# Performance work log

Measured on AMD Instinct MI355X. Metric: run time of the kernel, lower is better.

The kernel has to match this reference:

```python
import jax, jax.numpy as jnp
import numpy as np

N_NODES = 50000
N_EDGES = 600000
D_FEAT = 128
HIDDEN = 128
N_STEPS = 4


def setup_inputs() -> dict:
    key = jax.random.key(0)
    ks = jax.random.split(key, 10)
    node = jax.random.normal(ks[0], (N_NODES, D_FEAT), dtype=jnp.float32)
    edges = jax.random.randint(ks[1], (2, N_EDGES), 0, N_NODES, dtype=jnp.int64)
    edges_attr = jax.random.uniform(ks[2], (N_EDGES,), dtype=jnp.float32)
    s = 1.0 / np.sqrt(HIDDEN)
    W1 = jax.random.normal(ks[3], (D_FEAT, HIDDEN), dtype=jnp.float32) * s
    b1 = jnp.zeros((HIDDEN,), dtype=jnp.float32)
    Ws = jax.random.normal(ks[4], (N_STEPS, HIDDEN, HIDDEN), dtype=jnp.float32) * s
    bs = jnp.zeros((N_STEPS, HIDDEN), dtype=jnp.float32)
    Wfc = jax.random.normal(ks[5], (HIDDEN, 2), dtype=jnp.float32) * s
    bfc = jnp.zeros((2,), dtype=jnp.float32)
    return {"node": node, "edges": edges, "edges_attr": edges_attr,
            "W1": W1, "b1": b1, "Ws": Ws, "bs": bs, "Wfc": Wfc, "bfc": bfc}


def _gcn_norm(edges, edges_attr, n_nodes):
    # PyG gcn_norm with add_self_loops=True (fill 1.0)
    loop = jnp.arange(n_nodes, dtype=edges.dtype)
    row = jnp.concatenate([edges[0], loop])  # source
    col = jnp.concatenate([edges[1], loop])  # target
    ew = jnp.concatenate([edges_attr, jnp.ones((n_nodes,), dtype=edges_attr.dtype)])
    deg = jax.ops.segment_sum(ew, col, num_segments=n_nodes)
    dinv = jnp.where(deg > 0, jax.lax.rsqrt(jnp.where(deg > 0, deg, 1.0)), 0.0)
    norm = dinv[row] * ew * dinv[col]  # [E+N]
    return row, col, norm


def _gcn_conv(x, row, col, norm, W, b, n_nodes):
    h = x @ W                               # [N, H]
    msg = h[row] * norm[:, None]            # gather + scale [E+N, H]
    agg = jax.ops.segment_sum(msg, col, num_segments=n_nodes)  # scatter-add
    return agg + b


def reference(node, edges, edges_attr, W1, b1, Ws, bs, Wfc, bfc):
    n_nodes = node.shape[0]
    row, col, norm = _gcn_norm(edges, edges_attr, n_nodes)
    x = jax.nn.relu(_gcn_conv(node, row, col, norm, W1, b1, n_nodes))
    for i in range(Ws.shape[0]):
        x_res = x
        x = _gcn_conv(x, row, col, norm, Ws[i], bs[i], n_nodes)
        x = jax.nn.relu(x + x_res)  # residual=True
    x = x @ Wfc + bfc               # [N, 2]
    return jnp.mean(x, axis=0, keepdims=True)  # global_mean_pool(batch=None) -> [1, 2]
```

## Files before the change

kernel.cpp:

```cpp
#include <hip/hip_runtime.h>

#define N_NODES 50000
#define N_EDGES 600000
#define HID 128
#define NCOPY 8
#define NPART 3125

typedef __attribute__((ext_vector_type(8))) short bf16x8;
typedef __attribute__((ext_vector_type(8))) unsigned short u16x8;
typedef __attribute__((ext_vector_type(4))) float f32x4;
typedef __attribute__((ext_vector_type(2))) float f32x2;

__device__ __forceinline__ float bf2f(unsigned short u) {
    return __uint_as_float(((unsigned int)u) << 16);
}
__device__ __forceinline__ unsigned short f2bf(float f) {
    unsigned int u = __float_as_uint(f);
    u = (u + 0x7FFFu + ((u >> 16) & 1u)) >> 16;
    return (unsigned short)u;
}

__device__ __forceinline__ unsigned char fp8enc_hw(float f) {
    return (unsigned char)(__builtin_amdgcn_cvt_pk_fp8_f32(f, f, 0, false) & 0xff);
}


__global__ __launch_bounds__(256) void init_k(unsigned long long* degcnt8, float* cs,
                                              int2* epk_pad,
                                              const float* __restrict__ W1,
                                              const float* __restrict__ Ws,
                                              unsigned short* __restrict__ Wt_hi,
                                              unsigned short* __restrict__ Wt_lo,
                                              int total) {
    int i = blockIdx.x * 256 + threadIdx.x;
    if (i < total) degcnt8[i] = (i < N_NODES) ? (1ull << 32) : 0ull;
    if (i < HID) cs[i] = 0.0f;
    if (i < 8) epk_pad[i] = make_int2(0, 0);
    if (i < 5 * 16384) {
        int l = i >> 14;
        int r = i & 16383;
        int n = r >> 7;
        int k = r & 127;
        const float* src = (l == 0) ? W1 : (Ws + (size_t)(l - 1) * 16384);
        float w = src[k * 128 + n];
        unsigned short hi = f2bf(w);
        unsigned short lo = f2bf(w - bf2f(hi));
        Wt_hi[i] = hi;
        Wt_lo[i] = lo;
    }
}

__global__ __launch_bounds__(256) void edge_deg_k(const int* __restrict__ edges,
                                                  const float* __restrict__ attr,
                                                  unsigned long long* degcnt8,
                                                  int* __restrict__ rank) {
    int e = blockIdx.x * 256 + threadIdx.x;
    int copy = blockIdx.x & (NCOPY - 1);
    if (e < N_EDGES) {
        int c = edges[N_EDGES + e];
        unsigned long long enc = (1ull << 43) +
            (unsigned long long)llrintf(attr[e] * 4294967296.0f);
        unsigned long long old = atomicAdd(&degcnt8[(size_t)copy * N_NODES + c], enc);
        rank[e] = (int)(old >> 43);
    }
}

__global__ __launch_bounds__(256) void scan1_k(const unsigned long long* __restrict__ degcnt8,
                                               int* offs, int* bsum, float* dinv,
                                               int* __restrict__ cbase, int n) {
    __shared__ int s[256];
    int tid = threadIdx.x;
    int i = blockIdx.x * 256 + tid;
    int v = 0;
    if (i < n) {
        unsigned long long attrsum = 0;
        int running = 0;
        #pragma unroll
        for (int c = 0; c < NCOPY; ++c) {
            unsigned long long dc = degcnt8[(size_t)c * n + i];
            cbase[i * NCOPY + c] = running;
            running += (int)(dc >> 43);
            attrsum += dc & ((1ull << 43) - 1);
        }
        v = running;
        float deg = (float)attrsum * (1.0f / 4294967296.0f);
        dinv[i] = rsqrtf(deg);
    }
    s[tid] = v; __syncthreads();
    for (int d = 1; d < 256; d <<= 1) {
        int t = (tid >= d) ? s[tid - d] : 0;
        __syncthreads();
        s[tid] += t;
        __syncthreads();
    }
    if (i < n) offs[i] = s[tid] - v;
    if (tid == 255) bsum[blockIdx.x] = s[255];
}

__global__ __launch_bounds__(256) void scan3_k(int* offs, const int* __restrict__ bsum,
                                               int* cbase, int n, int nb) {
    __shared__ int s[256];
    int tid = threadIdx.x;
    int bv = (tid < nb) ? bsum[tid] : 0;
    s[tid] = bv; __syncthreads();
    for (int d = 1; d < 256; d <<= 1) {
        int t = (tid >= d) ? s[tid - d] : 0;
        __syncthreads();
        s[tid] += t;
        __syncthreads();
    }
    int b = blockIdx.x;
    int pbase = s[b] - bsum[b];
    int i = b * 256 + tid;
    if (i < n) {
        int v = offs[i] + pbase;
        offs[i] = v;
        #pragma unroll
        for (int c = 0; c < NCOPY; ++c) cbase[i * NCOPY + c] += v;
    }
}

__global__ __launch_bounds__(256) void fill_k(const int* __restrict__ edges,
                                              const float* __restrict__ attr,
                                              const float* __restrict__ dinv,
                                              const int* __restrict__ cbase,
                                              const int* __restrict__ rank,
                                              int2* __restrict__ epk) {
    int e = blockIdx.x * 256 + threadIdx.x;
    int copy = blockIdx.x & (NCOPY - 1);
    if (e < N_EDGES) {
        int r = edges[e];
        int c = edges[N_EDGES + e];
        float w = dinv[r] * attr[e] * dinv[c];
        epk[cbase[c * NCOPY + copy] + rank[e]] = make_int2(r, __float_as_int(w));
    }
}


template <bool FP32A>
__global__ __launch_bounds__(256) void mfma_gemm_k(const void* __restrict__ Av,
                                                   const unsigned short* __restrict__ Bh,
                                                   const unsigned short* __restrict__ Bl,
                                                   unsigned char* __restrict__ H, int nrows) {
    int wid  = threadIdx.x >> 6;
    int lane = threadIdx.x & 63;
    int row0 = blockIdx.x * 256 + wid * 64;
    int rl = lane & 15;
    int kg = lane >> 4;

    bf16x8 af[4][4];
    #pragma unroll
    for (int rt = 0; rt < 4; ++rt) {
        int row = row0 + rt * 16 + rl;
        int ar  = row < nrows ? row : nrows - 1;
        #pragma unroll
        for (int kt = 0; kt < 4; ++kt) {
            if (FP32A) {
                const float* Af = (const float*)Av;
                float4 v0 = *(const float4*)(Af + (size_t)ar * HID + kt * 32 + kg * 8);
                float4 v1 = *(const float4*)(Af + (size_t)ar * HID + kt * 32 + kg * 8 + 4);
                bf16x8 t;
                t[0] = (short)f2bf(v0.x); t[1] = (short)f2bf(v0.y);
                t[2] = (short)f2bf(v0.z); t[3] = (short)f2bf(v0.w);
                t[4] = (short)f2bf(v1.x); t[5] = (short)f2bf(v1.y);
                t[6] = (short)f2bf(v1.z); t[7] = (short)f2bf(v1.w);
                af[rt][kt] = t;
            } else {
                const unsigned short* Ab = (const unsigned short*)Av;
                af[rt][kt] = *(const bf16x8*)(Ab + (size_t)ar * HID + kt * 32 + kg * 8);
            }
        }
    }

    f32x4 acc[4][8];
    #pragma unroll
    for (int rt = 0; rt < 4; ++rt)
        #pragma unroll
        for (int nt = 0; nt < 8; ++nt) acc[rt][nt] = (f32x4){0.f, 0.f, 0.f, 0.f};

    #pragma unroll
    for (int nt = 0; nt < 8; ++nt) {
        #pragma unroll
        for (int kt = 0; kt < 4; ++kt) {
            size_t boff = (size_t)(nt * 16 + rl) * HID + kt * 32 + kg * 8;
            bf16x8 bh = *(const bf16x8*)(Bh + boff);
            bf16x8 bl = *(const bf16x8*)(Bl + boff);
            #pragma unroll
            for (int rt = 0; rt < 4; ++rt) {
                acc[rt][nt] = __builtin_amdgcn_mfma_f32_16x16x32_bf16(af[rt][kt], bh, acc[rt][nt], 0, 0, 0);
                acc[rt][nt] = __builtin_amdgcn_mfma_f32_16x16x32_bf16(af[rt][kt], bl, acc[rt][nt], 0, 0, 0);
            }
        }
    }

    #pragma unroll
    for (int rt = 0; rt < 4; ++rt) {
        #pragma unroll
        for (int nt = 0; nt < 8; ++nt) {
            #pragma unroll
            for (int r = 0; r < 4; ++r) {
                int orow = row0 + rt * 16 + kg * 4 + r;
                if (orow < nrows)
                    H[(size_t)orow * HID + nt * 16 + rl] = fp8enc_hw(acc[rt][nt][r]);
            }
        }
    }
}


__device__ __forceinline__ void dec_fma8_pk(uint2 q, float wt, f32x2* a) {
    f32x2 w2 = {wt, wt};
    a[0] += __builtin_amdgcn_cvt_pk_f32_fp8((int)q.x, false) * w2;
    a[1] += __builtin_amdgcn_cvt_pk_f32_fp8((int)q.x, true)  * w2;
    a[2] += __builtin_amdgcn_cvt_pk_f32_fp8((int)q.y, false) * w2;
    a[3] += __builtin_amdgcn_cvt_pk_f32_fp8((int)q.y, true)  * w2;
}

template <bool FINAL>
__global__ __launch_bounds__(256) void aggregate_k(const unsigned char* __restrict__ h,
                                                   const int* __restrict__ offs,
                                                   const int2* __restrict__ epk,
                                                   const float* __restrict__ dinv,
                                                   const float* __restrict__ bias,
                                                   const unsigned short* __restrict__ xprev,
                                                   unsigned short* __restrict__ xout,
                                                   float* __restrict__ part, int n) {
    int tid  = threadIdx.x;
    int wave = (blockIdx.x * 256 + tid) >> 6;
    int lane = tid & 63;
    int g  = lane >> 4;
    int ci = (lane & 15) * 8;
    int w = wave * 4 + g;
    int wc = w < n ? w : n - 1;

    f32x2 a[4];
    #pragma unroll
    for (int j = 0; j < 4; ++j) a[j] = (f32x2){0.f, 0.f};

    int e0 = 0, e1 = 0;
    if (w < n) {
        e0 = offs[w];
        e1 = (w + 1 < n) ? offs[w + 1] : N_EDGES;
    }

    for (int e = e0; e < e1; e += 8) {
        int2 pk[8];
        uint2 q[8];
        #pragma unroll
        for (int u = 0; u < 8; ++u) pk[u] = epk[e + u];
        #pragma unroll
        for (int u = 0; u < 8; ++u) {
            int row = (e + u < e1) ? pk[u].x : wc;
            q[u] = *(const uint2*)(h + (size_t)row * HID + ci);
        }
        #pragma unroll
        for (int u = 0; u < 8; ++u) {
            float wt = (e + u < e1) ? __int_as_float(pk[u].y) : 0.f;
            dec_fma8_pk(q[u], wt, a);
        }
    }

    float av[8];
    #pragma unroll
    for (int j = 0; j < 8; ++j) av[j] = 0.f;

    if (w < n) {
        float di = dinv[w];
        uint2 qw = *(const uint2*)(h + (size_t)w * HID + ci);
        dec_fma8_pk(qw, di * di, a);
        av[0] = a[0][0]; av[1] = a[0][1]; av[2] = a[1][0]; av[3] = a[1][1];
        av[4] = a[2][0]; av[5] = a[2][1]; av[6] = a[3][0]; av[7] = a[3][1];
        float4 b0 = *(const float4*)(bias + ci);
        float4 b1 = *(const float4*)(bias + ci + 4);
        av[0] += b0.x; av[1] += b0.y; av[2] += b0.z; av[3] += b0.w;
        av[4] += b1.x; av[5] += b1.y; av[6] += b1.z; av[7] += b1.w;
        if (xprev) {
            u16x8 xp = *(const u16x8*)(xprev + (size_t)w * HID + ci);
            #pragma unroll
            for (int j = 0; j < 8; ++j) av[j] += bf2f(xp[j]);
        }
        u16x8 o;
        #pragma unroll
        for (int j = 0; j < 8; ++j) {
            av[j] = fmaxf(av[j], 0.f);
            o[j] = f2bf(av[j]);
        }
        *(u16x8*)(xout + (size_t)w * HID + ci) = o;
    }

    if constexpr (FINAL) {
        #pragma unroll
        for (int j = 0; j < 8; ++j) av[j] += __shfl_xor(av[j], 16);
        #pragma unroll
        for (int j = 0; j < 8; ++j) av[j] += __shfl_xor(av[j], 32);
        __shared__ float sw[4][16][8];
        int wv = tid >> 6;
        if (lane < 16) {
            #pragma unroll
            for (int j = 0; j < 8; ++j) sw[wv][lane][j] = av[j];
        }
        __syncthreads();
        if (tid < 128) {
            int l16 = tid >> 3, j = tid & 7;
            part[(size_t)tid * NPART + blockIdx.x] =
                sw[0][l16][j] + sw[1][l16][j] + sw[2][l16][j] + sw[3][l16][j];
        }
    }
}


__global__ __launch_bounds__(256) void head_reduce_k(const float* __restrict__ part,
                                                     float* __restrict__ cs) {
    int col = blockIdx.x;
    float s = 0.f;
    for (int i = threadIdx.x; i < NPART; i += 256)
        s += part[(size_t)col * NPART + i];
    #pragma unroll
    for (int d = 1; d < 64; d <<= 1) s += __shfl_xor(s, d);
    __shared__ float sw[4];
    int lane = threadIdx.x & 63, wv = threadIdx.x >> 6;
    if (lane == 0) sw[wv] = s;
    __syncthreads();
    if (threadIdx.x == 0) cs[col] = sw[0] + sw[1] + sw[2] + sw[3];
}

__global__ __launch_bounds__(128) void final_k(const float* __restrict__ cs,
                                               const float* __restrict__ Wfc,
                                               const float* __restrict__ bfc,
                                               float* __restrict__ out) {
    __shared__ float s0[128], s1[128];
    int k = threadIdx.x;
    float c = cs[k];
    s0[k] = c * Wfc[k * 2 + 0];
    s1[k] = c * Wfc[k * 2 + 1];
    __syncthreads();
    for (int d = 64; d > 0; d >>= 1) {
        if (k < d) { s0[k] += s0[k + d]; s1[k] += s1[k + d]; }
        __syncthreads();
    }
    if (k == 0) {
        out[0] = s0[0] / (float)N_NODES + bfc[0];
        out[1] = s1[0] / (float)N_NODES + bfc[1];
    }
}


extern "C" void kernel_launch(void* const* d_in, const int* in_sizes, int n_in,
                              void* d_out, int out_size, void* d_ws, size_t ws_size,
                              hipStream_t stream) {
    const float* node  = (const float*)d_in[0];
    const int*   edges = (const int*)d_in[1];
    const float* attr  = (const float*)d_in[2];
    const float* W1    = (const float*)d_in[3];
    const float* b1    = (const float*)d_in[4];
    const float* Ws    = (const float*)d_in[5];
    const float* bs    = (const float*)d_in[6];
    const float* Wfc   = (const float*)d_in[7];
    const float* bfc   = (const float*)d_in[8];
    float* out = (float*)d_out;

    char* ws = (char*)d_ws;
    const size_t BN = (size_t)N_NODES * HID * 2;
    unsigned char*  h8     = (unsigned char*)(ws);
    unsigned short* xa_bf  = (unsigned short*)(ws + BN);
    unsigned short* xb_bf  = (unsigned short*)(ws + 2 * BN);
    char* p = ws + 3 * BN;
    unsigned long long* degcnt8 = (unsigned long long*)p; p += (size_t)NCOPY * N_NODES * 8;
    float* dinv  = (float*)p;            p += N_NODES * 4;
    int*   offs  = (int*)p;              p += N_NODES * 4;
    int*   cbase = (int*)p;              p += (size_t)N_NODES * NCOPY * 4;
    int*   rank  = (int*)p;              p += (size_t)N_EDGES * 4;
    int*   bsum  = (int*)p;              p += 1024;
    int2*  epk   = (int2*)p;             p += (size_t)(N_EDGES + 8) * 8;
    float* cs    = (float*)p;            p += 512;
    float* part  = (float*)p;            p += (size_t)128 * NPART * 4;
    unsigned short* wt_hi = (unsigned short*)p;  p += 5 * 16384 * 2;
    unsigned short* wt_lo = (unsigned short*)p;  p += 5 * 16384 * 2;

    const int NB_N  = (N_NODES + 255) / 256;
    const int NB_N8 = (NCOPY * N_NODES + 255) / 256;
    const int NB_E  = (N_EDGES + 255) / 256;

    hipLaunchKernelGGL(init_k,    dim3(NB_N8), dim3(256), 0, stream, degcnt8, cs,
                       epk + N_EDGES, W1, Ws, wt_hi, wt_lo, NCOPY * N_NODES);
    hipLaunchKernelGGL(edge_deg_k,dim3(NB_E),  dim3(256), 0, stream, edges, attr, degcnt8, rank);
    hipLaunchKernelGGL(scan1_k,   dim3(NB_N),  dim3(256), 0, stream, degcnt8, offs, bsum, dinv, cbase, N_NODES);
    hipLaunchKernelGGL(scan3_k,   dim3(NB_N),  dim3(256), 0, stream, offs, bsum, cbase, N_NODES, NB_N);
    hipLaunchKernelGGL(fill_k,    dim3(NB_E),  dim3(256), 0, stream, edges, attr, dinv, cbase, rank, epk);

    const int GB = (N_NODES + 255) / 256;
    const int AB = NPART;

    hipLaunchKernelGGL((mfma_gemm_k<true>), dim3(GB), dim3(256), 0, stream,
                       (const void*)node, wt_hi, wt_lo, h8, N_NODES);
    hipLaunchKernelGGL((aggregate_k<false>), dim3(AB), dim3(256), 0, stream, h8, offs, epk, dinv,
                       b1, (const unsigned short*)nullptr, xa_bf, part, N_NODES);

    unsigned short* xc = xa_bf;
    unsigned short* xn = xb_bf;
    for (int i = 0; i < 4; ++i) {
        hipLaunchKernelGGL((mfma_gemm_k<false>), dim3(GB), dim3(256), 0, stream,
                           (const void*)xc, wt_hi + (size_t)(i + 1) * 16384,
                           wt_lo + (size_t)(i + 1) * 16384, h8, N_NODES);
        if (i < 3) {
            hipLaunchKernelGGL((aggregate_k<false>), dim3(AB), dim3(256), 0, stream, h8, offs, epk, dinv,
                               bs + (size_t)i * HID, xc, xn, part, N_NODES);
        } else {
            hipLaunchKernelGGL((aggregate_k<true>), dim3(AB), dim3(256), 0, stream, h8, offs, epk, dinv,
                               bs + (size_t)i * HID, xc, xn, part, N_NODES);
        }
        unsigned short* t = xc; xc = xn; xn = t;
    }

    hipLaunchKernelGGL(head_reduce_k, dim3(128), dim3(256), 0, stream, part, cs);
    hipLaunchKernelGGL(final_k,       dim3(1),   dim3(128), 0, stream, cs, Wfc, bfc, out);
}
```

Baseline: 248.8 us.

## Degree-sort node processing order and pack edge records into 32 bits

```diff
diff --git a/kernel.cpp b/kernel.cpp
--- a/kernel.cpp
+++ b/kernel.cpp
@@ -1,4 +1,5 @@
 #include <hip/hip_runtime.h>
+#include <hip/hip_fp16.h>
 
 #define N_NODES 50000
 #define N_EDGES 600000
@@ -26,7 +27,7 @@
 
 
 __global__ __launch_bounds__(256) void init_k(unsigned long long* degcnt8, float* cs,
-                                              int2* epk_pad,
+                                              int* hist, unsigned* epk_pad,
                                               const float* __restrict__ W1,
                                               const float* __restrict__ Ws,
                                               unsigned short* __restrict__ Wt_hi,
@@ -35,7 +36,8 @@
     int i = blockIdx.x * 256 + threadIdx.x;
     if (i < total) degcnt8[i] = (i < N_NODES) ? (1ull << 32) : 0ull;
     if (i < HID) cs[i] = 0.0f;
-    if (i < 8) epk_pad[i] = make_int2(0, 0);
+    if (i < 256) hist[i] = 0;
+    if (i < 8) epk_pad[i] = 0u;
     if (i < 5 * 16384) {
         int l = i >> 14;
         int r = i & 16383;
@@ -67,7 +69,8 @@
 
 __global__ __launch_bounds__(256) void scan1_k(const unsigned long long* __restrict__ degcnt8,
                                                int* offs, int* bsum, float* dinv,
-                                               int* __restrict__ cbase, int n) {
+                                               int* __restrict__ cbase,
+                                               int* __restrict__ dcnt, int* hist, int n) {
     __shared__ int s[256];
     int tid = threadIdx.x;
     int i = blockIdx.x * 256 + tid;
@@ -85,6 +88,9 @@
         v = running;
         float deg = (float)attrsum * (1.0f / 4294967296.0f);
         dinv[i] = rsqrtf(deg);
+        int dcap = v < 255 ? v : 255;
+        dcnt[i] = dcap;
+        atomicAdd(&hist[dcap], 1);
     }
     s[tid] = v; __syncthreads();
     for (int d = 1; d < 256; d <<= 1) {
@@ -95,6 +101,29 @@
     }
     if (i < n) offs[i] = s[tid] - v;
     if (tid == 255) bsum[blockIdx.x] = s[255];
+}
+
+__global__ __launch_bounds__(256) void hist_scan_k(const int* __restrict__ hist, int* cursor) {
+    __shared__ int s[256];
+    int t = threadIdx.x;
+    int v = hist[t];
+    s[t] = v; __syncthreads();
+    for (int d = 1; d < 256; d <<= 1) {
+        int u = (t >= d) ? s[t - d] : 0;
+        __syncthreads();
+        s[t] += u;
+        __syncthreads();
+    }
+    cursor[t] = s[t] - v;
+}
+
+__global__ __launch_bounds__(256) void perm_k(const int* __restrict__ dcnt,
+                                              int* cursor, int* __restrict__ perm, int n) {
+    int i = blockIdx.x * 256 + threadIdx.x;
+    if (i < n) {
+        int p = atomicAdd(&cursor[dcnt[i]], 1);
+        perm[p] = i;
+    }
 }
 
 __global__ __launch_bounds__(256) void scan3_k(int* offs, const int* __restrict__ bsum,
@@ -125,14 +154,16 @@
                                               const float* __restrict__ dinv,
                                               const int* __restrict__ cbase,
                                               const int* __restrict__ rank,
-                                              int2* __restrict__ epk) {
+                                              unsigned* __restrict__ epk) {
     int e = blockIdx.x * 256 + threadIdx.x;
     int copy = blockIdx.x & (NCOPY - 1);
     if (e < N_EDGES) {
         int r = edges[e];
         int c = edges[N_EDGES + e];
         float w = dinv[r] * attr[e] * dinv[c];
-        epk[cbase[c * NCOPY + copy] + rank[e]] = make_int2(r, __float_as_int(w));
+        __half hw = __float2half(w);
+        unsigned pk = ((unsigned)__half_as_ushort(hw) << 16) | (unsigned)r;
+        epk[cbase[c * NCOPY + copy] + rank[e]] = pk;
     }
 }
 
@@ -219,9 +250,10 @@
 template <bool FINAL>
 __global__ __launch_bounds__(256) void aggregate_k(const unsigned char* __restrict__ h,
                                                    const int* __restrict__ offs,
-                                                   const int2* __restrict__ epk,
+                                                   const unsigned* __restrict__ epk,
                                                    const float* __restrict__ dinv,
                                                    const float* __restrict__ bias,
+                                                   const int* __restrict__ perm,
                                                    const unsigned short* __restrict__ xprev,
                                                    unsigned short* __restrict__ xout,
                                                    float* __restrict__ part, int n) {
@@ -230,8 +262,9 @@
     int lane = tid & 63;
     int g  = lane >> 4;
     int ci = (lane & 15) * 8;
-    int w = wave * 4 + g;
-    int wc = w < n ? w : n - 1;
+    int widx = wave * 4 + g;
+    int w = (widx < n) ? perm[widx] : n;
+    int wc = (w < n) ? w : 0;
 
     f32x2 a[4];
     #pragma unroll
@@ -244,18 +277,19 @@
     }
 
     for (int e = e0; e < e1; e += 8) {
-        int2 pk[8];
+        unsigned pk[8];
         uint2 q[8];
         #pragma unroll
         for (int u = 0; u < 8; ++u) pk[u] = epk[e + u];
         #pragma unroll
         for (int u = 0; u < 8; ++u) {
-            int row = (e + u < e1) ? pk[u].x : wc;
+            int row = (e + u < e1) ? (int)(pk[u] & 0xFFFFu) : wc;
             q[u] = *(const uint2*)(h + (size_t)row * HID + ci);
         }
         #pragma unroll
         for (int u = 0; u < 8; ++u) {
-            float wt = (e + u < e1) ? __int_as_float(pk[u].y) : 0.f;
+            float wt = (e + u < e1)
+                ? __half2float(__ushort_as_half((unsigned short)(pk[u] >> 16))) : 0.f;
             dec_fma8_pk(q[u], wt, a);
         }
     }
@@ -368,10 +402,14 @@
     unsigned long long* degcnt8 = (unsigned long long*)p; p += (size_t)NCOPY * N_NODES * 8;
     float* dinv  = (float*)p;            p += N_NODES * 4;
     int*   offs  = (int*)p;              p += N_NODES * 4;
+    int*   dcnt  = (int*)p;              p += N_NODES * 4;
+    int*   perm  = (int*)p;              p += N_NODES * 4;
     int*   cbase = (int*)p;              p += (size_t)N_NODES * NCOPY * 4;
     int*   rank  = (int*)p;              p += (size_t)N_EDGES * 4;
     int*   bsum  = (int*)p;              p += 1024;
-    int2*  epk   = (int2*)p;             p += (size_t)(N_EDGES + 8) * 8;
+    int*   hist  = (int*)p;              p += 1024;
+    int*   cursor= (int*)p;              p += 1024;
+    unsigned* epk = (unsigned*)p;        p += (size_t)(N_EDGES + 8) * 4;
     float* cs    = (float*)p;            p += 512;
     float* part  = (float*)p;            p += (size_t)128 * NPART * 4;
     unsigned short* wt_hi = (unsigned short*)p;  p += 5 * 16384 * 2;
@@ -381,12 +419,15 @@
     const int NB_N8 = (NCOPY * N_NODES + 255) / 256;
     const int NB_E  = (N_EDGES + 255) / 256;
 
-    hipLaunchKernelGGL(init_k,    dim3(NB_N8), dim3(256), 0, stream, degcnt8, cs,
+    hipLaunchKernelGGL(init_k,     dim3(NB_N8), dim3(256), 0, stream, degcnt8, cs, hist,
                        epk + N_EDGES, W1, Ws, wt_hi, wt_lo, NCOPY * N_NODES);
-    hipLaunchKernelGGL(edge_deg_k,dim3(NB_E),  dim3(256), 0, stream, edges, attr, degcnt8, rank);
-    hipLaunchKernelGGL(scan1_k,   dim3(NB_N),  dim3(256), 0, stream, degcnt8, offs, bsum, dinv, cbase, N_NODES);
-    hipLaunchKernelGGL(scan3_k,   dim3(NB_N),  dim3(256), 0, stream, offs, bsum, cbase, N_NODES, NB_N);
-    hipLaunchKernelGGL(fill_k,    dim3(NB_E),  dim3(256), 0, stream, edges, attr, dinv, cbase, rank, epk);
+    hipLaunchKernelGGL(edge_deg_k, dim3(NB_E),  dim3(256), 0, stream, edges, attr, degcnt8, rank);
+    hipLaunchKernelGGL(scan1_k,    dim3(NB_N),  dim3(256), 0, stream, degcnt8, offs, bsum, dinv,
+                       cbase, dcnt, hist, N_NODES);
+    hipLaunchKernelGGL(hist_scan_k,dim3(1),     dim3(256), 0, stream, hist, cursor);
+    hipLaunchKernelGGL(scan3_k,    dim3(NB_N),  dim3(256), 0, stream, offs, bsum, cbase, N_NODES, NB_N);
+    hipLaunchKernelGGL(perm_k,     dim3(NB_N),  dim3(256), 0, stream, dcnt, cursor, perm, N_NODES);
+    hipLaunchKernelGGL(fill_k,     dim3(NB_E),  dim3(256), 0, stream, edges, attr, dinv, cbase, rank, epk);
 
     const int GB = (N_NODES + 255) / 256;
     const int AB = NPART;
@@ -394,7 +435,7 @@
     hipLaunchKernelGGL((mfma_gemm_k<true>), dim3(GB), dim3(256), 0, stream,
                        (const void*)node, wt_hi, wt_lo, h8, N_NODES);
     hipLaunchKernelGGL((aggregate_k<false>), dim3(AB), dim3(256), 0, stream, h8, offs, epk, dinv,
-                       b1, (const unsigned short*)nullptr, xa_bf, part, N_NODES);
+                       b1, perm, (const unsigned short*)nullptr, xa_bf, part, N_NODES);
 
     unsigned short* xc = xa_bf;
     unsigned short* xn = xb_bf;
@@ -404,10 +445,10 @@
                            wt_lo + (size_t)(i + 1) * 16384, h8, N_NODES);
         if (i < 3) {
             hipLaunchKernelGGL((aggregate_k<false>), dim3(AB), dim3(256), 0, stream, h8, offs, epk, dinv,
-                               bs + (size_t)i * HID, xc, xn, part, N_NODES);
+                               bs + (size_t)i * HID, perm, xc, xn, part, N_NODES);
         } else {
             hipLaunchKernelGGL((aggregate_k<true>), dim3(AB), dim3(256), 0, stream, h8, offs, epk, dinv,
-                               bs + (size_t)i * HID, xc, xn, part, N_NODES);
+                               bs + (size_t)i * HID, perm, xc, xn, part, N_NODES);
         }
         unsigned short* t = xc; xc = xn; xn = t;
     }
```

Result: slower. 562.6 us (+126.1%).
